# Kernel tuning notes

Measured on AMD Instinct MI355X. Metric: run time of the kernel, lower is better.

## Reference

```python
import jax, jax.numpy as jnp
import numpy as np

C = 768      # n_embd
H = 12       # n_head
L = 6        # n_layer (per stack: base and head)
BS = 256     # block_size (per-stream length t)
B = 2        # batch
VU = 512     # vocab_size_up
VD = 512     # vocab_size_down
NM = 438     # n_music


def _ln(x, g, b, eps=1e-5):
    m = jnp.mean(x, -1, keepdims=True)
    v = jnp.mean((x - m) ** 2, -1, keepdims=True)
    return (x - m) * jax.lax.rsqrt(v + eps) * g + b


def _blocks(x, p, mask):
    # p: tuple of 16 stacked [L, ...] param arrays; scan over layers
    def body(x, lp):
        g1, b1, Wq, Bq, Wk, Bk, Wv, Bv, Wo, Bo, g2, b2, Wf, Bf, Wp, Bp = lp
        Bb, T, Cc = x.shape
        D = Cc // H
        h = _ln(x, g1, b1)
        q = (h @ Wq + Bq).reshape(Bb, T, H, D).transpose(0, 2, 1, 3)
        k = (h @ Wk + Bk).reshape(Bb, T, H, D).transpose(0, 2, 1, 3)
        v = (h @ Wv + Bv).reshape(Bb, T, H, D).transpose(0, 2, 1, 3)
        att = jnp.einsum('bhid,bhjd->bhij', q, k) * (1.0 / np.sqrt(D).astype(np.float32))
        att = jnp.where(mask, att, jnp.float32(-1e9))
        att = jax.nn.softmax(att, axis=-1)
        y = jnp.einsum('bhij,bhjd->bhid', att, v).transpose(0, 2, 1, 3).reshape(Bb, T, Cc)
        x = x + y @ Wo + Bo
        h2 = _ln(x, g2, b2)
        x = x + jax.nn.gelu(h2 @ Wf + Bf, approximate=False) @ Wp + Bp
        return x, None
    x, _ = jax.lax.scan(body, x, p)
    return x


def _forward(idx_up, idx_down, cond, tok_emb_up, tok_emb_down, pos_emb, cond_w, cond_b,
             base_p, head_p, ln_f_g, ln_f_b, head_up_w, head_down_w):
    t = idx_up.shape[1]
    te = jnp.concatenate([cond @ cond_w + cond_b, tok_emb_up[idx_up], tok_emb_down[idx_down]], axis=1)
    pe = jnp.concatenate([pos_emb[:, :t], pos_emb[:, BS:BS + t], pos_emb[:, 2 * BS:2 * BS + t]], axis=1)
    x = te + pe  # [B, 3t, C]
    tril = jnp.tril(jnp.ones((t, t), bool))
    mask = jnp.tile(tril, (3, 3))[None, None]  # 3x3 tiled block-causal mask [1,1,3t,3t]
    x = _blocks(x, base_p, mask)
    x = _blocks(x, head_p, mask)
    x = _ln(x, ln_f_g, ln_f_b)
    logits_up = x[:, t:2 * t] @ head_up_w
    logits_down = x[:, 2 * t:3 * t] @ head_down_w
    return logits_up, logits_down


def setup_inputs() -> dict:
    key = jax.random.key(0)
    ks = iter(jax.random.split(key, 100))
    def nrm(shape):
        return 0.02 * jax.random.normal(next(ks), shape, jnp.float32)
    inp = {
        'idx_up': jax.random.randint(next(ks), (B, BS), 0, VU),
        'idx_down': jax.random.randint(next(ks), (B, BS), 0, VD),
        'cond': jax.random.normal(next(ks), (B, BS, NM), jnp.float32),
        'tok_emb_up': nrm((VU, C)),
        'tok_emb_down': nrm((VD, C)),
        'pos_emb': nrm((1, 3 * BS, C)),
        'cond_w': nrm((NM, C)),
        'cond_b': jnp.zeros((C,), jnp.float32),
    }
    for pre in ('base_', 'head_'):
        inp[pre + 'ln1_g'] = jnp.ones((L, C), jnp.float32)
        inp[pre + 'ln1_b'] = jnp.zeros((L, C), jnp.float32)
        inp[pre + 'wq'] = nrm((L, C, C)); inp[pre + 'bq'] = jnp.zeros((L, C), jnp.float32)
        inp[pre + 'wk'] = nrm((L, C, C)); inp[pre + 'bk'] = jnp.zeros((L, C), jnp.float32)
        inp[pre + 'wv'] = nrm((L, C, C)); inp[pre + 'bv'] = jnp.zeros((L, C), jnp.float32)
        inp[pre + 'wo'] = nrm((L, C, C)); inp[pre + 'bo'] = jnp.zeros((L, C), jnp.float32)
        inp[pre + 'ln2_g'] = jnp.ones((L, C), jnp.float32)
        inp[pre + 'ln2_b'] = jnp.zeros((L, C), jnp.float32)
        inp[pre + 'fc_w'] = nrm((L, C, 4 * C)); inp[pre + 'fc_b'] = jnp.zeros((L, 4 * C), jnp.float32)
        inp[pre + 'pr_w'] = nrm((L, 4 * C, C)); inp[pre + 'pr_b'] = jnp.zeros((L, C), jnp.float32)
    inp['ln_f_g'] = jnp.ones((C,), jnp.float32)
    inp['ln_f_b'] = jnp.zeros((C,), jnp.float32)
    inp['head_up_w'] = nrm((C, VU))
    inp['head_down_w'] = nrm((C, VD))
    return inp


def reference(idx_up, idx_down, cond, tok_emb_up, tok_emb_down, pos_emb, cond_w, cond_b,
              base_ln1_g, base_ln1_b, base_wq, base_bq, base_wk, base_bk, base_wv, base_bv,
              base_wo, base_bo, base_ln2_g, base_ln2_b, base_fc_w, base_fc_b, base_pr_w, base_pr_b,
              head_ln1_g, head_ln1_b, head_wq, head_bq, head_wk, head_bk, head_wv, head_bv,
              head_wo, head_bo, head_ln2_g, head_ln2_b, head_fc_w, head_fc_b, head_pr_w, head_pr_b,
              ln_f_g, ln_f_b, head_up_w, head_down_w):
    base_p = (base_ln1_g, base_ln1_b, base_wq, base_bq, base_wk, base_bk, base_wv, base_bv,
              base_wo, base_bo, base_ln2_g, base_ln2_b, base_fc_w, base_fc_b, base_pr_w, base_pr_b)
    head_p = (head_ln1_g, head_ln1_b, head_wq, head_bq, head_wk, head_bk, head_wv, head_bv,
              head_wo, head_bo, head_ln2_g, head_ln2_b, head_fc_w, head_fc_b, head_pr_w, head_pr_b)
    return _forward(idx_up, idx_down, cond, tok_emb_up, tok_emb_down, pos_emb, cond_w, cond_b,
                    base_p, head_p, ln_f_g, ln_f_b, head_up_w, head_down_w)
```

## Files before the change

### kernel.cpp

```cpp
#include <hip/hip_runtime.h>
#include <cmath>

typedef unsigned short u16;
typedef __bf16 bf16x8 __attribute__((ext_vector_type(8)));
typedef float f32x4 __attribute__((ext_vector_type(4)));
typedef u16 u16x4 __attribute__((ext_vector_type(4)));
typedef u16 u16x2 __attribute__((ext_vector_type(2)));

#define GLOAD16(g, l) __builtin_amdgcn_global_load_lds( \
    (const __attribute__((address_space(1))) unsigned int*)(g), \
    (__attribute__((address_space(3))) unsigned int*)(l), 16, 0, 0)

__device__ __forceinline__ u16 f2b(float f) {
  unsigned u = __builtin_bit_cast(unsigned, f);
  unsigned r = (u + 0x7fffu + ((u >> 16) & 1u)) >> 16;
  return (u16)r;
}

__global__ __launch_bounds__(256)
void transw_k(const float* __restrict__ W, u16* __restrict__ Wt,
              int K, int N, int Kp, long sIn, long sOut)
{
  __shared__ float t[32][33];
  int n0 = blockIdx.x * 32, k0 = blockIdx.y * 32, l = blockIdx.z;
  const float* Wl = W + (long)l * sIn;
  u16* Wo = Wt + (long)l * sOut;
  int tx = threadIdx.x & 31, ty = threadIdx.x >> 5;
  #pragma unroll
  for (int i = 0; i < 4; ++i) {
    int k = k0 + ty + i * 8;
    t[ty + i * 8][tx] = (k < K) ? Wl[(long)k * N + n0 + tx] : 0.0f;
  }
  __syncthreads();
  #pragma unroll
  for (int i = 0; i < 2; ++i) {
    int p = threadIdx.x + 256 * i;
    int nl = p >> 4, kk = (p & 15) * 2;
    u16x2 o2; o2[0] = f2b(t[kk][nl]); o2[1] = f2b(t[kk + 1][nl]);
    *(u16x2*)(Wo + (long)(n0 + nl) * Kp + k0 + kk) = o2;
  }
}

__global__ void biascat_k(const float* bq0, const float* bk0, const float* bv0,
                          const float* bq1, const float* bk1, const float* bv1, float* o)
{
  int idx = blockIdx.x * 256 + threadIdx.x;
  int c = idx % 2304, l = idx / 2304;
  int st = l / 6, li = l % 6;
  const float* src = (c < 768) ? (st ? bq1 : bq0) : (c < 1536) ? (st ? bk1 : bk0) : (st ? bv1 : bv0);
  o[idx] = src[li * 768 + (c % 768)];
}

__global__ void condcvt_k(const float* __restrict__ c, u16* __restrict__ o)
{
  int idx = blockIdx.x * 256 + threadIdx.x;
  int k = idx % 448, r = idx / 448;
  o[idx] = f2b(k < 438 ? c[r * 438 + k] : 0.0f);
}

__global__ void embed_k(const int* __restrict__ iu, const int* __restrict__ idn,
                        const float* __restrict__ teu, const float* __restrict__ ted,
                        const float* __restrict__ pe, float* __restrict__ x)
{
  int idx = blockIdx.x * 256 + threadIdx.x;
  int c4 = idx % 192; int rest = idx / 192;
  int tt = rest % 512; int b = rest / 512;
  int i = tt & 255; int s = tt >> 8;
  int tok = s ? idn[b * 256 + i] : iu[b * 256 + i];
  const float4* src = (const float4*)(s ? (ted + (long)tok * 768) : (teu + (long)tok * 768));
  int prow = 256 + s * 256 + i;
  float4 pv = ((const float4*)(pe + (long)prow * 768))[c4];
  float4 sv = src[c4];
  float4 ov; ov.x = sv.x + pv.x; ov.y = sv.y + pv.y; ov.z = sv.z + pv.z; ov.w = sv.w + pv.w;
  ((float4*)(x + ((long)b * 768 + prow) * 768))[c4] = ov;
}

template<int S, bool WX>
__global__ __launch_bounds__(256)
void lnred_k(const float* __restrict__ xin, const float* __restrict__ P,
             const float* __restrict__ bias, const float* __restrict__ gg,
             const float* __restrict__ bb, float* __restrict__ xout,
             u16* __restrict__ h)
{
  int row = blockIdx.x * 4 + (threadIdx.x >> 6);
  int lane = threadIdx.x & 63;
  long base = (long)row * 768;
  float v[12]; float s = 0.0f;
  #pragma unroll
  for (int j = 0; j < 12; ++j) {
    int c = lane + 64 * j;
    float val = xin[base + c];
    if (S > 0) {
      val += bias[c];
      #pragma unroll
      for (int si = 0; si < S; ++si) val += P[(long)si * 1179648 + base + c];
    }
    if (WX) xout[base + c] = val;
    v[j] = val; s += val;
  }
  #pragma unroll
  for (int d = 1; d < 64; d <<= 1) s += __shfl_xor(s, d);
  float mean = s * (1.0f / 768.0f);
  float s2 = 0.0f;
  #pragma unroll
  for (int j = 0; j < 12; ++j) { float d = v[j] - mean; s2 += d * d; }
  #pragma unroll
  for (int d = 1; d < 64; d <<= 1) s2 += __shfl_xor(s2, d);
  float rstd = rsqrtf(s2 * (1.0f / 768.0f) + 1e-5f);
  u16* orow = h + base;
  #pragma unroll
  for (int j = 0; j < 12; ++j) {
    int c = lane + 64 * j;
    orow[c] = f2b((v[j] - mean) * rstd * gg[c] + bb[c]);
  }
}

__global__ __launch_bounds__(256)
void headred_k(const float* __restrict__ HP, float* __restrict__ out)
{
  int i4 = blockIdx.x * 256 + threadIdx.x;
  int st = i4 >> 16, loc = i4 & 65535;
  const float4* basep = (const float4*)HP + (long)st * 4 * 65536 + loc;
  float4 a = basep[0], b = basep[65536], c = basep[2 * 65536], d = basep[3 * 65536];
  float4 r; r.x = a.x + b.x + c.x + d.x; r.y = a.y + b.y + c.y + d.y;
  r.z = a.z + b.z + c.z + d.z; r.w = a.w + b.w + c.w + d.w;
  ((float4*)out)[i4] = r;
}

#define EPI_PLAIN 0
#define EPI_PE    1
#define EPI_QKV   2
#define EPI_GELU  4
#define EPI_PART  5

template<int BM, int BN, int WM, int WN, int EPI, bool BIAS>
__global__ __launch_bounds__(256)
void gemm_k(const u16* __restrict__ A, const u16* __restrict__ Bt, const float* __restrict__ bias,
            float* outf, u16* outb, u16* qb, u16* kb, u16* vT, const float* aux,
            int M, int N, int Ks, int lda, int ldb, int ldc,
            int astr, int aoff, int cstr, int coff, int pstr)
{
  constexpr int NWC = BN / WN;
  constexpr int NT  = (BM / WM) * NWC * 64;
  constexpr int LCH = (BM + BN) * 8;
  constexpr int LPT = LCH / NT;
  constexpr int MR = WM / 16, NR = WN / 16;
  __shared__ alignas(16) u16 Sl[2][(BM + BN) * 64];

  const int tid = threadIdx.x;
  const int m0 = blockIdx.x * BM, n0 = blockIdx.y * BN;
  const int koff = blockIdx.z * Ks;
  const int lane = tid & 63, w = tid >> 6, l15 = lane & 15, g = lane >> 4;
  const int wr = w / NWC, wc = w % NWC;

  const u16* gp[LPT]; int lbase[LPT];
  #pragma unroll
  for (int j = 0; j < LPT; ++j) {
    int c = tid + NT * j;
    int slot = c & 7;
    if (c < BM * 8) {
      int row = c >> 3;
      int se = (slot ^ (row & 7)) * 8;
      int am = m0 + row;
      gp[j] = A + (long)((am >> 8) * astr + aoff + (am & 255)) * lda + koff + se;
    } else {
      int rb = c - BM * 8;
      int row = rb >> 3;
      int se = (slot ^ (row & 7)) * 8;
      gp[j] = Bt + (long)(n0 + row) * ldb + koff + se;
    }
    lbase[j] = w * 512 + NT * 8 * j;
  }

  int offA[2][MR], offB[2][NR];
  #pragma unroll
  for (int ks = 0; ks < 2; ++ks) {
    int s = 4 * ks + g;
    #pragma unroll
    for (int mi = 0; mi < MR; ++mi) {
      int r = wr * WM + mi * 16 + l15;
      offA[ks][mi] = r * 128 + ((s ^ (r & 7)) << 4);
    }
    #pragma unroll
    for (int ni = 0; ni < NR; ++ni) {
      int r = wc * WN + ni * 16 + l15;
      offB[ks][ni] = BM * 128 + r * 128 + ((s ^ (r & 7)) << 4);
    }
  }

  f32x4 acc[MR][NR];
  #pragma unroll
  for (int mi = 0; mi < MR; ++mi)
  #pragma unroll
  for (int ni = 0; ni < NR; ++ni) acc[mi][ni] = f32x4{};

  auto STAGE = [&](int kt, int buf) {
    #pragma unroll
    for (int j = 0; j < LPT; ++j) GLOAD16(gp[j] + kt, &Sl[buf][lbase[j]]);
  };
  auto COMPUTE = [&](int buf) {
    const char* Sb = (const char*)&Sl[buf][0];
    #pragma unroll
    for (int ks = 0; ks < 2; ++ks) {
      bf16x8 a[MR], b[NR];
      #pragma unroll
      for (int mi = 0; mi < MR; ++mi) a[mi] = *(const bf16x8*)(Sb + offA[ks][mi]);
      #pragma unroll
      for (int ni = 0; ni < NR; ++ni) b[ni] = *(const bf16x8*)(Sb + offB[ks][ni]);
      #pragma unroll
      for (int mi = 0; mi < MR; ++mi)
      #pragma unroll
      for (int ni = 0; ni < NR; ++ni)
        acc[mi][ni] = __builtin_amdgcn_mfma_f32_16x16x32_bf16(a[mi], b[ni], acc[mi][ni], 0, 0, 0);
    }
  };

  const int nIter = Ks >> 6;
  STAGE(0, 0);
  if (nIter > 1) STAGE(64, 1);
  for (int t = 0; t < nIter; ++t) {
    if (t + 1 < nIter) {
      if constexpr (LPT == 8) asm volatile("s_waitcnt vmcnt(8)" ::: "memory");
      else                    asm volatile("s_waitcnt vmcnt(4)" ::: "memory");
    } else {
      asm volatile("s_waitcnt vmcnt(0)" ::: "memory");
    }
    __builtin_amdgcn_s_barrier();
    COMPUTE(t & 1);
    if (t + 2 < nIter) {
      __builtin_amdgcn_s_barrier();
      STAGE((t + 2) << 6, t & 1);
    }
  }

  #pragma unroll
  for (int mi = 0; mi < MR; ++mi)
  #pragma unroll
  for (int ni = 0; ni < NR; ++ni) {
    f32x4 a = acc[mi][ni];
    int col = n0 + wc * WN + ni * 16 + l15;
    float bv = BIAS ? bias[col] : 0.0f;
    int mlb = m0 + wr * WM + mi * 16 + 4 * g;
    if (EPI == EPI_QKV) {
      if (col >= 1536) {
        int c2 = col - 1536, hh = c2 >> 6, dd = c2 & 63;
        int bb2 = mlb >= 768 ? 1 : 0;
        int t0 = mlb - bb2 * 768;
        u16x4 pk;
        #pragma unroll
        for (int r = 0; r < 4; ++r) pk[r] = f2b(a[r] + bv);
        *(u16x4*)(vT + (long)((bb2 * 12 + hh) * 64 + dd) * 768 + t0) = pk;
      } else {
        u16* dst = (col < 768) ? (qb + (long)mlb * 768 + col) : (kb + (long)mlb * 768 + (col - 768));
        #pragma unroll
        for (int r = 0; r < 4; ++r) dst[(long)r * 768] = f2b(a[r] + bv);
      }
    } else {
      #pragma unroll
      for (int r = 0; r < 4; ++r) {
        int rg = mlb + r;
        long crow = (long)(rg >> 8) * cstr + coff + (rg & 255);
        float v = a[r] + bv;
        if (EPI == EPI_PLAIN)      outf[crow * ldc + col] = v;
        else if (EPI == EPI_PE)    outf[crow * ldc + col] = v + aux[(long)(rg & 255) * 768 + col];
        else if (EPI == EPI_PART)  outf[(long)blockIdx.z * pstr + (long)rg * ldc + col] = v;
        else if (EPI == EPI_GELU)  outb[crow * ldc + col] = f2b(0.5f * v * (1.0f + erff(v * 0.70710678f)));
      }
    }
  }
}

#define MFMA_BF16 __builtin_amdgcn_mfma_f32_16x16x32_bf16
__global__ __launch_bounds__(128)
void attn_k(const u16* __restrict__ qb, const u16* __restrict__ kb,
            const u16* __restrict__ vT, u16* __restrict__ y)
{
  __shared__ alignas(16) u16 Kl[3 * 4096];
  __shared__ alignas(16) u16 Vl[3 * 4096];
  __shared__ alignas(16) u16 Pl[2][16 * 72];
  const int qt = blockIdx.x, bh = blockIdx.y;
  const int b = bh / 12, h = bh - b * 12;
  const int tid = threadIdx.x, w = tid >> 6, lane = tid & 63, l15 = lane & 15, g = lane >> 4;
  const int qrow = qt * 32 + w * 16 + l15;
  const int qm = qrow & 255;
  const int q0 = (qt * 32) & 255;
  const unsigned nw4 = (q0 >> 6) + 1;
  const int niter = 3 * nw4;
  const u16* qp = qb + (long)(b * 768 + qrow) * 768 + h * 64;
  bf16x8 qf0 = *(const bf16x8*)(qp + 8 * g);
  bf16x8 qf1 = *(const bf16x8*)(qp + 32 + 8 * g);
  f32x4 O0{}, O1{}, O2{}, O3{};
  float m_run = -1e30f, l_run = 0.0f;

  const u16* kp[4]; const u16* vp[4]; int ldsb[4];
  #pragma unroll
  for (int j = 0; j < 4; ++j) {
    int i = tid + 128 * j;
    int r = i >> 3, sl = ((i & 7) ^ (r & 7)) * 8;
    kp[j] = kb + (long)(b * 768 + r) * 768 + h * 64 + sl;
    vp[j] = vT + (long)(bh * 64 + r) * 768 + sl;
    ldsb[j] = (w + 2 * j) * 512;
  }

  auto STAGE = [&](int kt, int q) {
    u16* kd = Kl + q * 4096; u16* vd = Vl + q * 4096;
    #pragma unroll
    for (int j = 0; j < 4; ++j) GLOAD16(kp[j] + (long)kt * 64 * 768, kd + ldsb[j]);
    #pragma unroll
    for (int j = 0; j < 4; ++j) GLOAD16(vp[j] + kt * 64, vd + ldsb[j]);
  };
  auto MAP = [&](int it) {
    unsigned sb = (unsigned)it / nw4;
    return (int)(sb * 4 + ((unsigned)it - sb * nw4));
  };

  STAGE(MAP(0), 0);
  STAGE(MAP(1), 1);
  int cur = 0;
  for (int it = 0; it < niter; ++it) {
    if (it < niter - 1) asm volatile("s_waitcnt vmcnt(8)" ::: "memory");
    else                asm volatile("s_waitcnt vmcnt(0)" ::: "memory");
    __builtin_amdgcn_s_barrier();
    if (it + 2 < niter) STAGE(MAP(it + 2), cur == 0 ? 2 : cur - 1);
    const int kt = MAP(it);
    const char* Kb = (const char*)Kl + cur * 8192;
    const char* Vb = (const char*)Vl + cur * 8192;

    f32x4 s0{}, s1{}, s2{}, s3{};
    #pragma unroll
    for (int ks = 0; ks < 2; ++ks) {
      bf16x8 qf = ks ? qf1 : qf0;
      int sb = ((4 * ks + g) ^ (l15 & 7)) << 4;
      bf16x8 k0 = *(const bf16x8*)(Kb + (0  + l15) * 128 + sb);
      bf16x8 k1 = *(const bf16x8*)(Kb + (16 + l15) * 128 + sb);
      bf16x8 k2 = *(const bf16x8*)(Kb + (32 + l15) * 128 + sb);
      bf16x8 k3 = *(const bf16x8*)(Kb + (48 + l15) * 128 + sb);
      s0 = MFMA_BF16(k0, qf, s0, 0, 0, 0);
      s1 = MFMA_BF16(k1, qf, s1, 0, 0, 0);
      s2 = MFMA_BF16(k2, qf, s2, 0, 0, 0);
      s3 = MFMA_BF16(k3, qf, s3, 0, 0, 0);
    }
    float sv[16]; float tm = -1e30f;
    #pragma unroll
    for (int mt = 0; mt < 4; ++mt) {
      f32x4 sm4 = (mt == 0) ? s0 : (mt == 1) ? s1 : (mt == 2) ? s2 : s3;
      #pragma unroll
      for (int r = 0; r < 4; ++r) {
        int kg = kt * 64 + mt * 16 + 4 * g + r;
        float val = ((kg & 255) <= qm) ? sm4[r] * 0.125f : -1e30f;
        sv[mt * 4 + r] = val; tm = fmaxf(tm, val);
      }
    }
    tm = fmaxf(tm, __shfl_xor(tm, 16));
    tm = fmaxf(tm, __shfl_xor(tm, 32));
    float mn = fmaxf(m_run, tm);
    float alpha = __expf(m_run - mn);
    float ps = 0.0f; u16 pb16[16];
    #pragma unroll
    for (int j = 0; j < 16; ++j) {
      float p = (sv[j] <= -1e29f) ? 0.0f : __expf(sv[j] - mn);
      ps += p; pb16[j] = f2b(p);
    }
    ps += __shfl_xor(ps, 16); ps += __shfl_xor(ps, 32);
    l_run = l_run * alpha + ps; m_run = mn;
    float a0 = __shfl(alpha, 4 * g + 0);
    float a1 = __shfl(alpha, 4 * g + 1);
    float a2 = __shfl(alpha, 4 * g + 2);
    float a3 = __shfl(alpha, 4 * g + 3);
    #pragma unroll
    for (int mt = 0; mt < 4; ++mt) {
      u16x4 pk; pk[0] = pb16[4*mt]; pk[1] = pb16[4*mt+1]; pk[2] = pb16[4*mt+2]; pk[3] = pb16[4*mt+3];
      *(u16x4*)((char*)&Pl[w][0] + l15 * 144 + mt * 32 + 8 * g) = pk;
    }
    O0[0] *= a0; O0[1] *= a1; O0[2] *= a2; O0[3] *= a3;
    O1[0] *= a0; O1[1] *= a1; O1[2] *= a2; O1[3] *= a3;
    O2[0] *= a0; O2[1] *= a1; O2[2] *= a2; O2[3] *= a3;
    O3[0] *= a0; O3[1] *= a1; O3[2] *= a2; O3[3] *= a3;
    asm volatile("s_waitcnt lgkmcnt(0)" ::: "memory");
    __builtin_amdgcn_sched_barrier(0);
    #pragma unroll
    for (int ks = 0; ks < 2; ++ks) {
      bf16x8 pf = *(const bf16x8*)((const char*)&Pl[w][0] + l15 * 144 + 64 * ks + 16 * g);
      int sb = ((4 * ks + g) ^ (l15 & 7)) << 4;
      bf16x8 v0 = *(const bf16x8*)(Vb + (0  + l15) * 128 + sb);
      bf16x8 v1 = *(const bf16x8*)(Vb + (16 + l15) * 128 + sb);
      bf16x8 v2 = *(const bf16x8*)(Vb + (32 + l15) * 128 + sb);
      bf16x8 v3 = *(const bf16x8*)(Vb + (48 + l15) * 128 + sb);
      O0 = MFMA_BF16(pf, v0, O0, 0, 0, 0);
      O1 = MFMA_BF16(pf, v1, O1, 0, 0, 0);
      O2 = MFMA_BF16(pf, v2, O2, 0, 0, 0);
      O3 = MFMA_BF16(pf, v3, O3, 0, 0, 0);
    }
    cur = (cur == 2) ? 0 : cur + 1;
  }
  float n0i = 1.0f / __shfl(l_run, 4 * g + 0);
  float n1i = 1.0f / __shfl(l_run, 4 * g + 1);
  float n2i = 1.0f / __shfl(l_run, 4 * g + 2);
  float n3i = 1.0f / __shfl(l_run, 4 * g + 3);
  long yr = (long)(b * 768 + qt * 32 + w * 16 + 4 * g);
  #pragma unroll
  for (int ni = 0; ni < 4; ++ni) {
    f32x4 Ov = (ni == 0) ? O0 : (ni == 1) ? O1 : (ni == 2) ? O2 : O3;
    int c = h * 64 + ni * 16 + l15;
    y[(yr + 0) * 768 + c] = f2b(Ov[0] * n0i);
    y[(yr + 1) * 768 + c] = f2b(Ov[1] * n1i);
    y[(yr + 2) * 768 + c] = f2b(Ov[2] * n2i);
    y[(yr + 3) * 768 + c] = f2b(Ov[3] * n3i);
  }
}

extern "C" void kernel_launch(void* const* d_in, const int* in_sizes, int n_in,
                              void* d_out, int out_size, void* d_ws, size_t ws_size,
                              hipStream_t stream)
{
  (void)in_sizes; (void)n_in; (void)out_size;
  auto F = [&](int i){ return (const float*)d_in[i]; };
  const int* idx_up = (const int*)d_in[0];
  const int* idx_dn = (const int*)d_in[1];
  const float* cond = F(2);
  const float* teu = F(3);
  const float* ted = F(4);
  const float* pe  = F(5);
  const float* cw  = F(6);
  const float* cb  = F(7);
  float* outp = (float*)d_out;
  char* ws = (char*)d_ws;

  size_t o = 0;
  auto take = [&](size_t bytes){ void* p = ws + o; o += bytes; return p; };
  float* x    = (float*)take(4718592);
  u16*   h    = (u16*)take(2359296);
  u16*   qbuf = (u16*)take(2359296);
  u16*   kbuf = (u16*)take(2359296);
  u16*   vT   = (u16*)take(2359296);
  u16*   y    = (u16*)take(2359296);
  u16*   fca  = (u16*)take(9437184);
  u16*   xf   = (u16*)take(2359296);
  u16*   cbf  = (u16*)take(458752);
  float* qkvb = (float*)take(110592);
  u16*   hut  = (u16*)take(786432);
  u16*   hdt  = (u16*)take(786432);
  u16*   cwt  = (u16*)take(688128);
  float* P1   = (float*)take(9437184);
  float* P2   = (float*)take(18874368);
  float* HP   = (float*)take(8388608);
  const size_t WL = 14155776;
  bool up = (ws_size >= o + 12 * WL);
  size_t nsl = up ? 12 : 1;
  u16* qkvt = (u16*)(ws + o);
  u16* wot  = qkvt + nsl * 2304 * 768;
  u16* fct  = wot  + nsl * 768 * 768;
  u16* prt  = fct  + nsl * 3072 * 768;

  auto trans = [&](const float* src, u16* dst, int K, int N, int Kp, long sIn, long sOut, int nz){
    transw_k<<<dim3(N / 32, Kp / 32, nz), dim3(256), 0, stream>>>(src, dst, K, N, Kp, sIn, sOut);
  };

  if (up) {
    for (int s = 0; s < 2; ++s) {
      for (int p = 0; p < 3; ++p)
        trans(F(8 + 16*s + 2 + 2*p), qkvt + (size_t)s*6*2304*768 + (size_t)p*768*768,
              768, 768, 768, 768L*768, 2304L*768, 6);
      trans(F(8 + 16*s + 8),  wot + (size_t)s*6*768*768,  768, 768, 768, 768L*768, 768L*768, 6);
      trans(F(8 + 16*s + 12), fct + (size_t)s*6*3072*768, 768, 3072, 768, 768L*3072, 3072L*768, 6);
      trans(F(8 + 16*s + 14), prt + (size_t)s*6*768*3072, 3072, 768, 3072, 3072L*768, 768L*3072, 6);
    }
  }
  trans(F(42), hut, 768, 512, 768, 0, 0, 1);
  trans(F(43), hdt, 768, 512, 768, 0, 0, 1);
  trans(cw,    cwt, 438, 768, 448, 0, 0, 1);
  biascat_k<<<dim3(108), dim3(256), 0, stream>>>(F(11), F(13), F(15), F(27), F(29), F(31), qkvb);
  condcvt_k<<<dim3(896), dim3(256), 0, stream>>>(cond, cbf);
  embed_k<<<dim3(768), dim3(256), 0, stream>>>(idx_up, idx_dn, teu, ted, pe, x);
  gemm_k<64, 64, 32, 32, EPI_PE, true><<<dim3(8, 12, 1), dim3(256), 0, stream>>>(cbf, cwt, cb,
      x, nullptr, nullptr, nullptr, nullptr, pe,
      512, 768, 448, 448, 448, 768, 256, 0, 768, 0, 0);

  for (int l = 0; l < 12; ++l) {
    int s = l / 6, li = l % 6;
    u16* qkvt_l = qkvt + (up ? (size_t)l : 0) * 2304 * 768;
    u16* wot_l  = wot  + (up ? (size_t)l : 0) * 768 * 768;
    u16* fct_l  = fct  + (up ? (size_t)l : 0) * 3072 * 768;
    u16* prt_l  = prt  + (up ? (size_t)l : 0) * 768 * 3072;
    if (!up) {
      for (int p = 0; p < 3; ++p)
        trans(F(8 + 16*s + 2 + 2*p) + (size_t)li*768*768, qkvt_l + (size_t)p*768*768, 768, 768, 768, 0, 0, 1);
      trans(F(8 + 16*s + 8)  + (size_t)li*768*768,  wot_l, 768, 768, 768, 0, 0, 1);
      trans(F(8 + 16*s + 12) + (size_t)li*768*3072, fct_l, 768, 3072, 768, 0, 0, 1);
      trans(F(8 + 16*s + 14) + (size_t)li*3072*768, prt_l, 3072, 768, 3072, 0, 0, 1);
    }
    if (l == 0) {
      lnred_k<0, false><<<dim3(384), dim3(256), 0, stream>>>(x, nullptr, nullptr,
          F(8+16*s+0) + (size_t)li*768, F(8+16*s+1) + (size_t)li*768, nullptr, h);
    } else {
      int ps = (l - 1) / 6, pli = (l - 1) % 6;
      lnred_k<4, true><<<dim3(384), dim3(256), 0, stream>>>(x, P2,
          F(8+16*ps+15) + (size_t)pli*768,
          F(8+16*s+0) + (size_t)li*768, F(8+16*s+1) + (size_t)li*768, x, h);
    }
    gemm_k<128, 128, 64, 64, EPI_QKV, true><<<dim3(12, 18, 1), dim3(256), 0, stream>>>(h, qkvt_l, qkvb + (size_t)l*2304,
        nullptr, nullptr, qbuf, kbuf, vT, nullptr,
        1536, 2304, 768, 768, 768, 768, 256, 0, 256, 0, 0);
    attn_k<<<dim3(24, 24), dim3(128), 0, stream>>>(qbuf, kbuf, vT, y);
    gemm_k<128, 128, 64, 64, EPI_PART, false><<<dim3(12, 6, 2), dim3(256), 0, stream>>>(y, wot_l, nullptr,
        P1, nullptr, nullptr, nullptr, nullptr, nullptr,
        1536, 768, 384, 768, 768, 768, 256, 0, 256, 0, 1179648);
    lnred_k<2, true><<<dim3(384), dim3(256), 0, stream>>>(x, P1,
        F(8+16*s+9) + (size_t)li*768,
        F(8+16*s+10) + (size_t)li*768, F(8+16*s+11) + (size_t)li*768, x, h);
    gemm_k<128, 128, 64, 64, EPI_GELU, true><<<dim3(12, 24, 1), dim3(256), 0, stream>>>(h, fct_l, F(8+16*s+13) + (size_t)li*3072,
        nullptr, fca, nullptr, nullptr, nullptr, nullptr,
        1536, 3072, 768, 768, 768, 3072, 256, 0, 256, 0, 0);
    gemm_k<128, 128, 64, 64, EPI_PART, false><<<dim3(12, 6, 4), dim3(256), 0, stream>>>(fca, prt_l, nullptr,
        P2, nullptr, nullptr, nullptr, nullptr, nullptr,
        1536, 768, 768, 3072, 3072, 768, 256, 0, 256, 0, 1179648);
  }
  lnred_k<4, false><<<dim3(384), dim3(256), 0, stream>>>(x, P2,
      F(8+16*1+15) + (size_t)5*768, F(40), F(41), nullptr, xf);
  gemm_k<64, 64, 32, 32, EPI_PART, false><<<dim3(8, 8, 4), dim3(256), 0, stream>>>(xf, hut, nullptr,
      HP, nullptr, nullptr, nullptr, nullptr, nullptr,
      512, 512, 192, 768, 768, 512, 768, 256, 256, 0, 262144);
  gemm_k<64, 64, 32, 32, EPI_PART, false><<<dim3(8, 8, 4), dim3(256), 0, stream>>>(xf, hdt, nullptr,
      HP + 1048576, nullptr, nullptr, nullptr, nullptr, nullptr,
      512, 512, 192, 768, 768, 512, 768, 512, 256, 0, 262144);
  headred_k<<<dim3(512), dim3(256), 0, stream>>>(HP, outp);
}
```

Before: 1.419 ms.

## Swizzle workgroups across XCDs and vectorize layernorm loads/stores

```diff
diff --git a/kernel.cpp b/kernel.cpp
--- a/kernel.cpp
+++ b/kernel.cpp
@@ -15,6 +15,12 @@
   unsigned u = __builtin_bit_cast(unsigned, f);
   unsigned r = (u + 0x7fffu + ((u >> 16) & 1u)) >> 16;
   return (u16)r;
+}
+
+__device__ __forceinline__ int xcd_swz(int lin, int nwg) {
+  int q = nwg >> 3, r = nwg & 7;
+  int xcd = lin & 7, idx = lin >> 3;
+  return xcd * q + (xcd < r ? xcd : r) + idx;
 }
 
 __global__ __launch_bounds__(256)
@@ -85,33 +91,48 @@
   int row = blockIdx.x * 4 + (threadIdx.x >> 6);
   int lane = threadIdx.x & 63;
   long base = (long)row * 768;
-  float v[12]; float s = 0.0f;
-  #pragma unroll
-  for (int j = 0; j < 12; ++j) {
-    int c = lane + 64 * j;
-    float val = xin[base + c];
+  const float4* xr4 = (const float4*)(xin + base);
+  float4 v[3]; float s = 0.0f;
+  #pragma unroll
+  for (int j = 0; j < 3; ++j) {
+    int f = lane + 64 * j;
+    float4 val = xr4[f];
     if (S > 0) {
-      val += bias[c];
-      #pragma unroll
-      for (int si = 0; si < S; ++si) val += P[(long)si * 1179648 + base + c];
-    }
-    if (WX) xout[base + c] = val;
-    v[j] = val; s += val;
+      float4 bv = ((const float4*)bias)[f];
+      val.x += bv.x; val.y += bv.y; val.z += bv.z; val.w += bv.w;
+      #pragma unroll
+      for (int si = 0; si < S; ++si) {
+        float4 pv = ((const float4*)(P + (long)si * 1179648 + base))[f];
+        val.x += pv.x; val.y += pv.y; val.z += pv.z; val.w += pv.w;
+      }
+    }
+    if (WX) ((float4*)(xout + base))[f] = val;
+    v[j] = val; s += val.x + val.y + val.z + val.w;
   }
   #pragma unroll
   for (int d = 1; d < 64; d <<= 1) s += __shfl_xor(s, d);
   float mean = s * (1.0f / 768.0f);
   float s2 = 0.0f;
   #pragma unroll
-  for (int j = 0; j < 12; ++j) { float d = v[j] - mean; s2 += d * d; }
+  for (int j = 0; j < 3; ++j) {
+    float dx = v[j].x - mean, dy = v[j].y - mean, dz = v[j].z - mean, dw = v[j].w - mean;
+    s2 += dx * dx + dy * dy + dz * dz + dw * dw;
+  }
   #pragma unroll
   for (int d = 1; d < 64; d <<= 1) s2 += __shfl_xor(s2, d);
   float rstd = rsqrtf(s2 * (1.0f / 768.0f) + 1e-5f);
   u16* orow = h + base;
   #pragma unroll
-  for (int j = 0; j < 12; ++j) {
-    int c = lane + 64 * j;
-    orow[c] = f2b((v[j] - mean) * rstd * gg[c] + bb[c]);
+  for (int j = 0; j < 3; ++j) {
+    int f = lane + 64 * j;
+    float4 gv = ((const float4*)gg)[f];
+    float4 bv2 = ((const float4*)bb)[f];
+    u16x4 pk;
+    pk[0] = f2b((v[j].x - mean) * rstd * gv.x + bv2.x);
+    pk[1] = f2b((v[j].y - mean) * rstd * gv.y + bv2.y);
+    pk[2] = f2b((v[j].z - mean) * rstd * gv.z + bv2.z);
+    pk[3] = f2b((v[j].w - mean) * rstd * gv.w + bv2.w);
+    *(u16x4*)(orow + 4 * f) = pk;
   }
 }
 
@@ -148,8 +169,14 @@
   __shared__ alignas(16) u16 Sl[2][(BM + BN) * 64];
 
   const int tid = threadIdx.x;
-  const int m0 = blockIdx.x * BM, n0 = blockIdx.y * BN;
-  const int koff = blockIdx.z * Ks;
+  const int gx = gridDim.x, gy = gridDim.y;
+  const int nwg = gx * gy * gridDim.z;
+  const int lin = (blockIdx.z * gy + blockIdx.y) * gx + blockIdx.x;
+  const int wg = xcd_swz(lin, nwg);
+  const int bx = wg % gx, t1g = wg / gx;
+  const int by = t1g % gy, bz = t1g / gy;
+  const int m0 = bx * BM, n0 = by * BN;
+  const int koff = bz * Ks;
   const int lane = tid & 63, w = tid >> 6, l15 = lane & 15, g = lane >> 4;
   const int wr = w / NWC, wc = w % NWC;
 
@@ -263,7 +290,7 @@
         float v = a[r] + bv;
         if (EPI == EPI_PLAIN)      outf[crow * ldc + col] = v;
         else if (EPI == EPI_PE)    outf[crow * ldc + col] = v + aux[(long)(rg & 255) * 768 + col];
-        else if (EPI == EPI_PART)  outf[(long)blockIdx.z * pstr + (long)rg * ldc + col] = v;
+        else if (EPI == EPI_PART)  outf[(long)bz * pstr + (long)rg * ldc + col] = v;
         else if (EPI == EPI_GELU)  outb[crow * ldc + col] = f2b(0.5f * v * (1.0f + erff(v * 0.70710678f)));
       }
     }
@@ -278,7 +305,11 @@
   __shared__ alignas(16) u16 Kl[3 * 4096];
   __shared__ alignas(16) u16 Vl[3 * 4096];
   __shared__ alignas(16) u16 Pl[2][16 * 72];
-  const int qt = blockIdx.x, bh = blockIdx.y;
+  const int gx = gridDim.x, gy = gridDim.y;
+  const int nwg = gx * gy;
+  const int lin = blockIdx.y * gx + blockIdx.x;
+  const int wg = xcd_swz(lin, nwg);
+  const int qt = wg % gx, bh = wg / gx;
   const int b = bh / 12, h = bh - b * 12;
   const int tid = threadIdx.x, w = tid >> 6, lane = tid & 63, l15 = lane & 15, g = lane >> 4;
   const int qrow = qt * 32 + w * 16 + l15;
```

Result: faster. 1.354 ms (-4.6%).
